# Kernel optimization log

Hardware: AMD Instinct MI355X
Metric: run time of the kernel (lower is better)

Reference implementation:

```python
import jax, jax.numpy as jnp
import numpy as np


def setup_inputs() -> dict:
    key = jax.random.key(0)
    k_x, k_rbf, k_nb, k_w1, k_w2 = jax.random.split(key, 5)
    N, NB, F_DIM, RBF_DIM = 20000, 32, 128, 64
    x = jax.random.normal(k_x, (N, F_DIM), dtype=jnp.float32)
    rbf = jax.random.uniform(k_rbf, (N, NB, RBF_DIM), dtype=jnp.float32)
    neighbors = jax.random.randint(k_nb, (N, NB), 0, N, dtype=jnp.int64)
    # filter network params (Linear(rbf_dim->f_dim), Softplus, Linear(f_dim->f_dim))
    w1 = jax.random.normal(k_w1, (RBF_DIM, F_DIM), dtype=jnp.float32) / np.sqrt(RBF_DIM)
    b1 = jnp.zeros((F_DIM,), dtype=jnp.float32)
    w2 = jax.random.normal(k_w2, (F_DIM, F_DIM), dtype=jnp.float32) / np.sqrt(F_DIM)
    b2 = jnp.zeros((F_DIM,), dtype=jnp.float32)
    return {"x": x, "rbf": rbf, "neighbors": neighbors,
            "w1": w1, "b1": b1, "w2": w2, "b2": b2}


def reference(x, rbf, neighbors, w1, b1, w2, b2):
    # filter network: Linear -> Softplus -> Linear, applied per (atom, neighbor)
    h = jax.nn.softplus(jnp.einsum('anr,rf->anf', rbf, w1) + b1)  # [N, NB, F]
    W = jnp.einsum('ang,gf->anf', h, w2) + b2                      # [N, NB, F]
    x_j = x[neighbors]                                             # gather [N, NB, F]
    return jnp.sum(x_j * W, axis=1)                                # [N, F]
```

## Files before the change

kernel.cpp:

```cpp
#include <hip/hip_runtime.h>
#include <hip/hip_bf16.h>
#include <math.h>


#define NB     32
#define FD     128
#define RD     64
#define WAVES  8
#define NTILES 2500

#define LOG2E 1.4426950408889634f
#define LN2   0.6931471805599453f

typedef short  short8  __attribute__((ext_vector_type(8)));
typedef float  floatx4 __attribute__((ext_vector_type(4)));
typedef float  floatx2 __attribute__((ext_vector_type(2)));
typedef int    intx4   __attribute__((ext_vector_type(4)));

#define LDS_FENCE() asm volatile("" ::: "memory")

static __device__ __forceinline__ unsigned pk2(float a, float b) {
  __hip_bfloat162 h = __float22bfloat162_rn(float2{a, b});
  unsigned u;
  __builtin_memcpy(&u, &h, sizeof(u));
  return u;
}

static __device__ __forceinline__ float sp2(float acc) {
  return __builtin_amdgcn_logf(1.0f + __builtin_amdgcn_exp2f(acc));
}

__global__ __launch_bounds__(512, 2)
void cfconv_kernel(const float* __restrict__ x,
                   const float* __restrict__ rbf,
                   const int*   __restrict__ nbr,
                   const float* __restrict__ w1,
                   const float* __restrict__ b1,
                   const float* __restrict__ w2,
                   const float* __restrict__ b2,
                   float* __restrict__ out) {
  __shared__ __align__(16) short w1f[16][64][8];
  __shared__ __align__(16) short w2f[32][64][8];
  __shared__ __align__(16) unsigned long long hb[WAVES][16][32];

  const int tid  = threadIdx.x;
  const int lane = tid & 63;
  const int wv   = tid >> 6;
  const int q    = lane >> 4;
  const int ln   = lane & 15;

  for (int i = tid; i < RD * FD; i += 512) {
    int k = i >> 7, n = i & 127, kk = k & 31;
    w1f[(k >> 5) * 8 + (n >> 4)][(kk >> 3) * 16 + (n & 15)][kk & 7] =
        (short)pk2(w1[i] * LOG2E, 0.f);
  }
  for (int i = tid; i < FD * FD; i += 512) {
    int k = i >> 7, n = i & 127, kk = k & 31;
    w2f[(k >> 5) * 8 + (n >> 4)][(kk >> 3) * 16 + (n & 15)][kk & 7] =
        (short)pk2(w2[i] * LN2, 0.f);
  }
  __syncthreads();

  unsigned long long (*band)[32] = hb[wv];
  const int swz = ln ^ ((ln & 2) << 3);

  for (int tile = blockIdx.x; tile < NTILES; tile += gridDim.x) {
    const int atom = tile * WAVES + wv;
    const int prow = atom * NB;
    const int* nbp = nbr + prow;

    float o[8];
#pragma unroll
    for (int nt = 0; nt < 8; ++nt) o[nt] = 0.f;

#pragma unroll
    for (int mt = 0; mt < 2; ++mt) {
      const intx4 nbi = *(const intx4*)(nbp + mt * 16 + q * 4);

      floatx4 acc[8];

      {
        const float* src = rbf + (size_t)(prow + mt * 16 + ln) * RD + q * 8;
        short8 bfr[2];
#pragma unroll
        for (int kt = 0; kt < 2; ++kt) {
          floatx4 lo = __builtin_nontemporal_load((const floatx4*)(src + kt * 32));
          floatx4 hi = __builtin_nontemporal_load((const floatx4*)(src + kt * 32 + 4));
          union { short8 s8; unsigned u[4]; } f;
          f.u[0] = pk2(lo[0], lo[1]);
          f.u[1] = pk2(lo[2], lo[3]);
          f.u[2] = pk2(hi[0], hi[1]);
          f.u[3] = pk2(hi[2], hi[3]);
          bfr[kt] = f.s8;
        }

#pragma unroll
        for (int nt = 0; nt < 8; ++nt) {
          floatx4 bv = *(const floatx4*)(b1 + nt * 16 + q * 4);
          acc[nt] = floatx4{bv[0] * LOG2E, bv[1] * LOG2E, bv[2] * LOG2E, bv[3] * LOG2E};
        }
#pragma unroll
        for (int kt = 0; kt < 2; ++kt)
#pragma unroll
          for (int nt = 0; nt < 8; ++nt) {
            short8 afr = *(const short8*)&w1f[kt * 8 + nt][lane][0];
            acc[nt] = __builtin_amdgcn_mfma_f32_16x16x32_bf16(afr, bfr[kt], acc[nt], 0, 0, 0);
          }
      }

#pragma unroll
      for (int nt = 0; nt < 8; ++nt) {
        unsigned u0 = pk2(sp2(acc[nt][0]), sp2(acc[nt][1]));
        unsigned u1 = pk2(sp2(acc[nt][2]), sp2(acc[nt][3]));
        unsigned long long v = (unsigned long long)u0 | ((unsigned long long)u1 << 32);
        band[ln][(nt * 4 + q) ^ swz] = v;
      }
      LDS_FENCE();

      const float* xb0 = x + (size_t)nbi[0] * FD + ln;
      float xa[8], xc[8];
#pragma unroll
      for (int nt = 0; nt < 8; ++nt) xa[nt] = xb0[nt * 16];

#pragma unroll
      for (int nt = 0; nt < 8; ++nt) {
        float bb = b2[nt * 16 + ln];
        acc[nt] = floatx4{bb, bb, bb, bb};
      }
#pragma unroll
      for (int kt = 0; kt < 4; ++kt) {
        union { short8 s8; unsigned long long d[2]; } f;
        f.d[0] = band[ln][(kt * 8 + q * 2)     ^ swz];
        f.d[1] = band[ln][(kt * 8 + q * 2 + 1) ^ swz];
        const short8 hk = f.s8;
#pragma unroll
        for (int nt = 0; nt < 8; ++nt) {
          short8 bfr2 = *(const short8*)&w2f[kt * 8 + nt][lane][0];
          acc[nt] = __builtin_amdgcn_mfma_f32_16x16x32_bf16(hk, bfr2, acc[nt], 0, 0, 0);
        }
      }
      LDS_FENCE();

      const float* xb1 = x + (size_t)nbi[1] * FD + ln;
#pragma unroll
      for (int nt = 0; nt < 8; ++nt) xc[nt] = xb1[nt * 16];
#pragma unroll
      for (int nt = 0; nt < 8; ++nt) o[nt] = fmaf(xa[nt], acc[nt][0], o[nt]);

      const float* xb2 = x + (size_t)nbi[2] * FD + ln;
#pragma unroll
      for (int nt = 0; nt < 8; ++nt) xa[nt] = xb2[nt * 16];
#pragma unroll
      for (int nt = 0; nt < 8; ++nt) o[nt] = fmaf(xc[nt], acc[nt][1], o[nt]);

      const float* xb3 = x + (size_t)nbi[3] * FD + ln;
#pragma unroll
      for (int nt = 0; nt < 8; ++nt) xc[nt] = xb3[nt * 16];
#pragma unroll
      for (int nt = 0; nt < 8; ++nt) o[nt] = fmaf(xa[nt], acc[nt][2], o[nt]);

#pragma unroll
      for (int nt = 0; nt < 8; ++nt) o[nt] = fmaf(xc[nt], acc[nt][3], o[nt]);
    }

#pragma unroll
    for (int nt = 0; nt < 8; ++nt) {
      o[nt] += __shfl_xor(o[nt], 16);
      o[nt] += __shfl_xor(o[nt], 32);
    }
    float s0 = o[0], s1 = o[1];
    if (q == 1) { s0 = o[2]; s1 = o[3]; }
    if (q == 2) { s0 = o[4]; s1 = o[5]; }
    if (q == 3) { s0 = o[6]; s1 = o[7]; }
    float* op = out + (size_t)atom * FD + q * 32 + ln;
    __builtin_nontemporal_store(s0, op);
    __builtin_nontemporal_store(s1, op + 16);
  }
}

extern "C" void kernel_launch(void* const* d_in, const int* in_sizes, int n_in,
                              void* d_out, int out_size, void* d_ws, size_t ws_size,
                              hipStream_t stream) {
  const float* x   = (const float*)d_in[0];
  const float* rbf = (const float*)d_in[1];
  const int*   nbr = (const int*)d_in[2];
  const float* w1  = (const float*)d_in[3];
  const float* b1  = (const float*)d_in[4];
  const float* w2  = (const float*)d_in[5];
  const float* b2  = (const float*)d_in[6];
  float* out = (float*)d_out;

  cfconv_kernel<<<dim3(500), dim3(512), 0, stream>>>(x, rbf, nbr, w1, b1, w2, b2, out);
}
```

Before: 312.5 us.

## Switch to 32x32x16 MFMA with register-resident hidden layer and rbf prefetch

Replaces the 16x16x32 MFMA pipeline with 32x32x16 MFMAs computing one atom's 32 neighbors per wave. The softplus hidden activations are passed into the second GEMM through cross-half lane shuffles instead of an LDS staging buffer. The next tile's rbf rows are prefetched into registers while the current tile computes. Blocks shrink to 4 waves with a larger grid. This raises register pressure, and the gather of neighbor x rows is now serialized over 16 rows per lane.

```diff
diff --git a/kernel.cpp b/kernel.cpp
--- a/kernel.cpp
+++ b/kernel.cpp
@@ -6,8 +6,8 @@
 #define NB     32
 #define FD     128
 #define RD     64
-#define WAVES  8
-#define NTILES 2500
+#define WPB    4
+#define NTILES 5000
 
 #define LOG2E 1.4426950408889634f
 #define LN2   0.6931471805599453f
@@ -15,9 +15,9 @@
 typedef short  short8  __attribute__((ext_vector_type(8)));
 typedef float  floatx4 __attribute__((ext_vector_type(4)));
 typedef float  floatx2 __attribute__((ext_vector_type(2)));
-typedef int    intx4   __attribute__((ext_vector_type(4)));
+typedef float  f32x16  __attribute__((ext_vector_type(16)));
 
-#define LDS_FENCE() asm volatile("" ::: "memory")
+#define NTLOAD(p) __builtin_nontemporal_load((const floatx4*)(p))
 
 static __device__ __forceinline__ unsigned pk2(float a, float b) {
   __hip_bfloat162 h = __float22bfloat162_rn(float2{a, b});
@@ -30,7 +30,7 @@
   return __builtin_amdgcn_logf(1.0f + __builtin_amdgcn_exp2f(acc));
 }
 
-__global__ __launch_bounds__(512, 2)
+__global__ __launch_bounds__(256, 3)
 void cfconv_kernel(const float* __restrict__ x,
                    const float* __restrict__ rbf,
                    const int*   __restrict__ nbr,
@@ -39,142 +39,131 @@
                    const float* __restrict__ w2,
                    const float* __restrict__ b2,
                    float* __restrict__ out) {
-  __shared__ __align__(16) short w1f[16][64][8];
+  __shared__ __align__(16) short w1t[16][64][8];
   __shared__ __align__(16) short w2f[32][64][8];
-  __shared__ __align__(16) unsigned long long hb[WAVES][16][32];
 
   const int tid  = threadIdx.x;
   const int lane = tid & 63;
   const int wv   = tid >> 6;
-  const int q    = lane >> 4;
-  const int ln   = lane & 15;
+  const int c    = lane & 31;
+  const int hi   = lane >> 5;
 
-  for (int i = tid; i < RD * FD; i += 512) {
-    int k = i >> 7, n = i & 127, kk = k & 31;
-    w1f[(k >> 5) * 8 + (n >> 4)][(kk >> 3) * 16 + (n & 15)][kk & 7] =
+  for (int i = tid; i < RD * FD; i += 256) {
+    int r = i >> 7, f = i & 127;
+    w1t[(f >> 5) * 4 + (r >> 4)][((r >> 3) & 1) * 32 + (f & 31)][r & 7] =
         (short)pk2(w1[i] * LOG2E, 0.f);
   }
-  for (int i = tid; i < FD * FD; i += 512) {
-    int k = i >> 7, n = i & 127, kk = k & 31;
-    w2f[(k >> 5) * 8 + (n >> 4)][(kk >> 3) * 16 + (n & 15)][kk & 7] =
+  for (int i = tid; i < FD * FD; i += 256) {
+    int k = i >> 7, n = i & 127;
+    w2f[(k >> 4) * 4 + (n >> 5)][((k >> 3) & 1) * 32 + (n & 31)][k & 7] =
         (short)pk2(w2[i] * LN2, 0.f);
   }
+  float b2v[4];
+#pragma unroll
+  for (int nt = 0; nt < 4; ++nt) b2v[nt] = b2[nt * 32 + c];
   __syncthreads();
 
-  unsigned long long (*band)[32] = hb[wv];
-  const int swz = ln ^ ((ln & 2) << 3);
+  floatx4 nxt[8];
+  {
+    const float* s = rbf + (size_t)((blockIdx.x * WPB + wv) * NB + c) * RD + hi * 8;
+#pragma unroll
+    for (int kt = 0; kt < 4; ++kt) {
+      nxt[2 * kt]     = NTLOAD(s + kt * 16);
+      nxt[2 * kt + 1] = NTLOAD(s + kt * 16 + 4);
+    }
+  }
 
   for (int tile = blockIdx.x; tile < NTILES; tile += gridDim.x) {
-    const int atom = tile * WAVES + wv;
+    const int atom = tile * WPB + wv;
     const int prow = atom * NB;
-    const int* nbp = nbr + prow;
 
-    float o[8];
+    short8 bfr[4];
 #pragma unroll
-    for (int nt = 0; nt < 8; ++nt) o[nt] = 0.f;
+    for (int kt = 0; kt < 4; ++kt) {
+      floatx4 lo = nxt[2 * kt], hq = nxt[2 * kt + 1];
+      union { short8 s8; unsigned u[4]; } fu;
+      fu.u[0] = pk2(lo[0], lo[1]);
+      fu.u[1] = pk2(lo[2], lo[3]);
+      fu.u[2] = pk2(hq[0], hq[1]);
+      fu.u[3] = pk2(hq[2], hq[3]);
+      bfr[kt] = fu.s8;
+    }
+
+    f32x16 acc2[4];
+#pragma unroll
+    for (int nt = 0; nt < 4; ++nt)
+#pragma unroll
+      for (int e = 0; e < 16; ++e) acc2[nt][e] = b2v[nt];
 
 #pragma unroll
-    for (int mt = 0; mt < 2; ++mt) {
-      const intx4 nbi = *(const intx4*)(nbp + mt * 16 + q * 4);
+    for (int mt = 0; mt < 4; ++mt) {
+      floatx2 b1p[8];
+#pragma unroll
+      for (int p = 0; p < 8; ++p)
+        b1p[p] = *(const floatx2*)(b1 + mt * 32 + hi * 4 + (p & 1) * 2 + (p >> 1) * 8);
 
-      floatx4 acc[8];
+      f32x16 acc1 = {};
+#pragma unroll
+      for (int kt = 0; kt < 4; ++kt) {
+        short8 afr = *(const short8*)&w1t[mt * 4 + kt][lane][0];
+        acc1 = __builtin_amdgcn_mfma_f32_32x32x16_bf16(afr, bfr[kt], acc1, 0, 0, 0);
+      }
 
-      {
-        const float* src = rbf + (size_t)(prow + mt * 16 + ln) * RD + q * 8;
-        short8 bfr[2];
+      unsigned pw[8], qw[8];
 #pragma unroll
-        for (int kt = 0; kt < 2; ++kt) {
-          floatx4 lo = __builtin_nontemporal_load((const floatx4*)(src + kt * 32));
-          floatx4 hi = __builtin_nontemporal_load((const floatx4*)(src + kt * 32 + 4));
-          union { short8 s8; unsigned u[4]; } f;
-          f.u[0] = pk2(lo[0], lo[1]);
-          f.u[1] = pk2(lo[2], lo[3]);
-          f.u[2] = pk2(hi[0], hi[1]);
-          f.u[3] = pk2(hi[2], hi[3]);
-          bfr[kt] = f.s8;
-        }
+      for (int p = 0; p < 8; ++p)
+        pw[p] = pk2(sp2(acc1[2 * p] + b1p[p][0]), sp2(acc1[2 * p + 1] + b1p[p][1]));
+#pragma unroll
+      for (int p = 0; p < 8; ++p)
+        qw[p] = (unsigned)__shfl_xor((int)pw[p], 32, 64);
 
 #pragma unroll
-        for (int nt = 0; nt < 8; ++nt) {
-          floatx4 bv = *(const floatx4*)(b1 + nt * 16 + q * 4);
-          acc[nt] = floatx4{bv[0] * LOG2E, bv[1] * LOG2E, bv[2] * LOG2E, bv[3] * LOG2E};
+      for (int s = 0; s < 2; ++s) {
+        union { short8 s8; unsigned u[4]; } a2;
+        a2.u[0] = hi ? qw[4 * s + 2] : pw[4 * s];
+        a2.u[1] = hi ? qw[4 * s + 3] : pw[4 * s + 1];
+        a2.u[2] = hi ? pw[4 * s + 2] : qw[4 * s];
+        a2.u[3] = hi ? pw[4 * s + 3] : qw[4 * s + 1];
+#pragma unroll
+        for (int nt = 0; nt < 4; ++nt) {
+          short8 bf2 = *(const short8*)&w2f[(2 * mt + s) * 4 + nt][lane][0];
+          acc2[nt] = __builtin_amdgcn_mfma_f32_32x32x16_bf16(a2.s8, bf2, acc2[nt], 0, 0, 0);
         }
-#pragma unroll
-        for (int kt = 0; kt < 2; ++kt)
-#pragma unroll
-          for (int nt = 0; nt < 8; ++nt) {
-            short8 afr = *(const short8*)&w1f[kt * 8 + nt][lane][0];
-            acc[nt] = __builtin_amdgcn_mfma_f32_16x16x32_bf16(afr, bfr[kt], acc[nt], 0, 0, 0);
-          }
       }
+    }
 
-#pragma unroll
-      for (int nt = 0; nt < 8; ++nt) {
-        unsigned u0 = pk2(sp2(acc[nt][0]), sp2(acc[nt][1]));
-        unsigned u1 = pk2(sp2(acc[nt][2]), sp2(acc[nt][3]));
-        unsigned long long v = (unsigned long long)u0 | ((unsigned long long)u1 << 32);
-        band[ln][(nt * 4 + q) ^ swz] = v;
-      }
-      LDS_FENCE();
-
-      const float* xb0 = x + (size_t)nbi[0] * FD + ln;
-      float xa[8], xc[8];
-#pragma unroll
-      for (int nt = 0; nt < 8; ++nt) xa[nt] = xb0[nt * 16];
-
-#pragma unroll
-      for (int nt = 0; nt < 8; ++nt) {
-        float bb = b2[nt * 16 + ln];
-        acc[nt] = floatx4{bb, bb, bb, bb};
-      }
+    {
+      int tnext = tile + gridDim.x;
+      if (tnext >= NTILES) tnext = tile;
+      const float* s = rbf + (size_t)((tnext * WPB + wv) * NB + c) * RD + hi * 8;
 #pragma unroll
       for (int kt = 0; kt < 4; ++kt) {
-        union { short8 s8; unsigned long long d[2]; } f;
-        f.d[0] = band[ln][(kt * 8 + q * 2)     ^ swz];
-        f.d[1] = band[ln][(kt * 8 + q * 2 + 1) ^ swz];
-        const short8 hk = f.s8;
-#pragma unroll
-        for (int nt = 0; nt < 8; ++nt) {
-          short8 bfr2 = *(const short8*)&w2f[kt * 8 + nt][lane][0];
-          acc[nt] = __builtin_amdgcn_mfma_f32_16x16x32_bf16(hk, bfr2, acc[nt], 0, 0, 0);
-        }
+        nxt[2 * kt]     = NTLOAD(s + kt * 16);
+        nxt[2 * kt + 1] = NTLOAD(s + kt * 16 + 4);
       }
-      LDS_FENCE();
-
-      const float* xb1 = x + (size_t)nbi[1] * FD + ln;
-#pragma unroll
-      for (int nt = 0; nt < 8; ++nt) xc[nt] = xb1[nt * 16];
-#pragma unroll
-      for (int nt = 0; nt < 8; ++nt) o[nt] = fmaf(xa[nt], acc[nt][0], o[nt]);
-
-      const float* xb2 = x + (size_t)nbi[2] * FD + ln;
-#pragma unroll
-      for (int nt = 0; nt < 8; ++nt) xa[nt] = xb2[nt * 16];
-#pragma unroll
-      for (int nt = 0; nt < 8; ++nt) o[nt] = fmaf(xc[nt], acc[nt][1], o[nt]);
-
-      const float* xb3 = x + (size_t)nbi[3] * FD + ln;
-#pragma unroll
-      for (int nt = 0; nt < 8; ++nt) xc[nt] = xb3[nt * 16];
-#pragma unroll
-      for (int nt = 0; nt < 8; ++nt) o[nt] = fmaf(xa[nt], acc[nt][2], o[nt]);
-
-#pragma unroll
-      for (int nt = 0; nt < 8; ++nt) o[nt] = fmaf(xc[nt], acc[nt][3], o[nt]);
     }
 
+    const int* nbp = nbr + prow;
+    float o[4] = {0.f, 0.f, 0.f, 0.f};
 #pragma unroll
-    for (int nt = 0; nt < 8; ++nt) {
-      o[nt] += __shfl_xor(o[nt], 16);
-      o[nt] += __shfl_xor(o[nt], 32);
+    for (int rr = 0; rr < 16; ++rr) {
+      const int row = (rr & 3) + 8 * (rr >> 2) + 4 * hi;
+      const int j   = nbp[row];
+      const float* xp = x + (size_t)j * FD + c;
+      float xv0 = xp[0], xv1 = xp[32], xv2 = xp[64], xv3 = xp[96];
+      o[0] = fmaf(xv0, acc2[0][rr], o[0]);
+      o[1] = fmaf(xv1, acc2[1][rr], o[1]);
+      o[2] = fmaf(xv2, acc2[2][rr], o[2]);
+      o[3] = fmaf(xv3, acc2[3][rr], o[3]);
     }
-    float s0 = o[0], s1 = o[1];
-    if (q == 1) { s0 = o[2]; s1 = o[3]; }
-    if (q == 2) { s0 = o[4]; s1 = o[5]; }
-    if (q == 3) { s0 = o[6]; s1 = o[7]; }
-    float* op = out + (size_t)atom * FD + q * 32 + ln;
+#pragma unroll
+    for (int nt = 0; nt < 4; ++nt) o[nt] += __shfl_xor(o[nt], 32, 64);
+
+    float s0 = hi ? o[2] : o[0];
+    float s1 = hi ? o[3] : o[1];
+    float* op = out + (size_t)atom * FD + hi * 64 + c;
     __builtin_nontemporal_store(s0, op);
-    __builtin_nontemporal_store(s1, op + 16);
+    __builtin_nontemporal_store(s1, op + 32);
   }
 }
 
@@ -190,5 +179,5 @@
   const float* b2  = (const float*)d_in[6];
   float* out = (float*)d_out;
 
-  cfconv_kernel<<<dim3(500), dim3(512), 0, stream>>>(x, rbf, nbr, w1, b1, w2, b2, out);
+  cfconv_kernel<<<dim3(1250), dim3(256), 0, stream>>>(x, rbf, nbr, w1, b1, w2, b2, out);
 }
```

Result: slower. 677.9 us (+116.9%).
